# Performance work log

Hardware: AMD Instinct MI355X
Metric: run time of the kernel (lower is better)

## Reference

```python
import jax, jax.numpy as jnp
import numpy as np

PI = 3.141592653589793
DET_THRESHOLD = 0.25
MAX_DET = 100
REG_HEAD = 4
DEPTH_MEAN = 28.01  # smoke_coder.depth_ref[0]
DIM_REF = (3.88, 1.63, 1.53)  # smoke_coder.dim_ref[0] (l, h, w)


def setup_inputs() -> dict:
    key = jax.random.key(0)
    k1, k2, k3, k4 = jax.random.split(key, 4)
    B, C, H, W = 32, 3, 256, 832  # stride-4 feature map of 3328x1024 images
    pred_heatmap = jax.random.uniform(k1, (B, C, H, W), dtype=jnp.float32)
    pred_regression = jax.random.normal(k2, (B, C + 1, H, W), dtype=jnp.float32) * 0.1  # REG_HEAD=4 channels
    trans_mat = jnp.tile(jnp.array([[0.25, 0.0, 0.0], [0.0, 0.25, 0.0], [0.0, 0.0, 1.0]], jnp.float32), (B, 1, 1))
    K_mat = jnp.tile(jnp.array([[2100.0, 0.0, 1664.0], [0.0, 2100.0, 512.0], [0.0, 0.0, 1.0]], jnp.float32), (B, 1, 1))
    size = jnp.tile(jnp.array([3328.0, 1024.0], jnp.float32), (B, 1))  # (img_w, img_h)
    h_cam = jax.random.uniform(k3, (B,), jnp.float32, 1.4, 2.0)
    dimensions = jax.random.uniform(k4, (B, 3), jnp.float32, 1.5, 4.0)
    return dict(pred_heatmap=pred_heatmap, pred_regression=pred_regression, trans_mat=trans_mat,
                K_mat=K_mat, size=size, h_cam=h_cam, dimensions=dimensions)


def reference(pred_heatmap, pred_regression, trans_mat, K_mat, size, h_cam, dimensions):
    B, C, H, W = pred_heatmap.shape
    K = MAX_DET
    # ---- nms_hm: 3x3 max-pool, keep local maxima ----
    hmax = jax.lax.reduce_window(pred_heatmap, -jnp.inf, jax.lax.max, (1, 1, 3, 3), (1, 1, 1, 1), 'SAME')
    heat = pred_heatmap * (hmax == pred_heatmap).astype(pred_heatmap.dtype)
    # ---- select_topk: per-class topk then global topk ----
    scores_c, inds_c = jax.lax.top_k(heat.reshape(B, C, H * W), K)  # [B,C,K]
    ys_c = (inds_c // W).astype(jnp.float32)
    xs_c = (inds_c % W).astype(jnp.float32)
    scores, topk_ind = jax.lax.top_k(scores_c.reshape(B, C * K), K)  # [B,K]
    clses = (topk_ind // K).astype(jnp.float32)
    inds = jnp.take_along_axis(inds_c.reshape(B, C * K), topk_ind, axis=1)
    ys = jnp.take_along_axis(ys_c.reshape(B, C * K), topk_ind, axis=1)
    xs = jnp.take_along_axis(xs_c.reshape(B, C * K), topk_ind, axis=1)
    feat = pred_regression.reshape(B, REG_HEAD, H * W).transpose(0, 2, 1)  # [B,HW,R]
    pois = jnp.take_along_axis(feat, inds[:, :, None], axis=1).reshape(-1, REG_HEAD)  # [B*K,R]
    log_dv_delta = pois[:, 0]
    off_u = pois[:, 1]
    ori = pois[:, 2:]
    # ---- feature points -> image points via inverse affine ----
    pts = jnp.stack([xs.reshape(-1), ys.reshape(-1)], axis=1)
    pts = pts + jnp.stack([off_u, jnp.zeros_like(off_u)], axis=1)
    pts_h = jnp.concatenate([pts, jnp.ones((pts.shape[0], 1), pts.dtype)], axis=1)  # [N,3]
    obj = jnp.repeat(jnp.arange(B), K)
    trans_inv = jnp.linalg.inv(trans_mat)[obj]  # [N,3,3]
    img_pts = jnp.einsum('nij,nj->ni', trans_inv, pts_h)[:, :2]
    # ---- per-object camera params ----
    Ks = K_mat[obj]
    h = h_cam[obj]
    kd = dimensions[obj]
    fx, fy, cx = Ks[:, 0, 0], Ks[:, 1, 1], Ks[:, 0, 2]
    dim_ref = jnp.array(DIM_REF, jnp.float32)
    dims = jnp.where(jnp.isfinite(kd), kd, dim_ref[None, :])
    # ---- geometric depth decode ----
    h_ref = h - dims[:, 1] / 2.0
    log_dv_ref = jnp.log(jnp.clip(fy * jnp.abs(h_ref), 1e-7, None) / DEPTH_MEAN)
    log_dv = jnp.clip(log_dv_ref + log_dv_delta, -4.0, 8.0)
    depths = jnp.clip(fy * jnp.abs(h_ref) * jnp.exp(-log_dv), 0.5, 120.0)
    px = (img_pts[:, 0] - cx) * depths / fx
    locs = jnp.stack([px, h, depths], axis=1)  # [N,3]
    # ---- decode_orientation (SMOKE) ----
    rays = jnp.arctan(locs[:, 0] / (locs[:, 2] + 1e-7))
    alphas = jnp.arctan(ori[:, 0] / (ori[:, 1] + 1e-7))
    alphas = alphas + jnp.where(ori[:, 1] >= 0, -PI / 2, PI / 2)
    rotys = alphas + rays
    rotys = jnp.where(rotys > PI, rotys - 2 * PI, rotys)
    rotys = jnp.where(rotys < -PI, rotys + 2 * PI, rotys)
    # ---- encode_box2d: build 3D corners, rotate, project, clamp ----
    cos, sin = jnp.cos(rotys), jnp.sin(rotys)
    cx8 = jnp.array([-0.5, 0.5, 0.5, 0.5, 0.5, -0.5, -0.5, -0.5], jnp.float32)
    cy8 = jnp.array([-1.0, -1.0, 0.0, 0.0, -1.0, -1.0, 0.0, 0.0], jnp.float32)
    cz8 = jnp.array([-0.5, -0.5, -0.5, 0.5, 0.5, 0.5, 0.5, -0.5], jnp.float32)
    xc = dims[:, 0:1] * cx8  # l
    yc = dims[:, 1:2] * cy8  # h
    zc = dims[:, 2:3] * cz8  # w
    bx = cos[:, None] * xc + sin[:, None] * zc
    bz = -sin[:, None] * xc + cos[:, None] * zc
    box3d = jnp.stack([bx, yc, bz], axis=1) + locs[:, :, None]  # [N,3,8]
    proj = jnp.einsum('nij,njk->nik', Ks, box3d)
    uv = proj[:, :2, :] / proj[:, 2:3, :]
    img_w = size.reshape(-1)[0]
    img_h = size.reshape(-1)[1]
    xmins = jnp.clip(jnp.min(uv[:, 0, :], axis=1), 0.0, img_w)
    xmaxs = jnp.clip(jnp.max(uv[:, 0, :], axis=1), 0.0, img_w)
    ymins = jnp.clip(jnp.min(uv[:, 1, :], axis=1), 0.0, img_h)
    ymaxs = jnp.clip(jnp.max(uv[:, 1, :], axis=1), 0.0, img_h)
    box2d = jnp.stack([xmins, ymins, xmaxs, ymaxs], axis=1)
    pred_dims = jnp.roll(dims, -1, axis=1)  # (l,h,w)->(h,w,l)
    result = jnp.concatenate([clses.reshape(-1, 1), alphas[:, None], box2d, pred_dims, locs,
                              rotys[:, None], scores.reshape(-1, 1)], axis=1)  # [N,14]
    # fixed-shape equivalent of boolean filtering: zero out rows below threshold
    keep = (result[:, -1] > DET_THRESHOLD).astype(result.dtype)
    return result * keep[:, None]
```

## Files before the change

kernel.cpp:

```cpp
#include <hip/hip_runtime.h>
#include <math.h>

#define B_ 32
#define C_ 3
#define H_ 256
#define W_ 832
#define HW_ (H_*W_)
#define NQ (W_/4)
#define K_ 100
#define RPB 16
#define PARTS (H_/RPB)
#define BLK 256
#define CAP 2048
#define NCAND (C_*PARTS*K_)
#define NB 2048
#define TIE_CAP 128
#define SEL_PASSES 6
#define QPW 62

typedef unsigned long long ull;

template<int N>
__device__ inline void bitonic_sort_desc(ull* s) {
    for (int k = 2; k <= N; k <<= 1) {
        for (int j = k >> 1; j > 0; j >>= 1) {
            __syncthreads();
            for (int i = threadIdx.x; i < N; i += BLK) {
                int ixj = i ^ j;
                if (ixj > i) {
                    ull a = s[i], b = s[ixj];
                    bool up = ((i & k) == 0);
                    if (up ? (a < b) : (a > b)) { s[i] = b; s[ixj] = a; }
                }
            }
        }
    }
    __syncthreads();
}

__device__ inline void find_digit(const unsigned* __restrict__ hist,
                                  unsigned* __restrict__ wtot,
                                  const int kneed,
                                  int* __restrict__ d_s,
                                  int* __restrict__ krem_s,
                                  int* __restrict__ m_s) {
    const int tid = threadIdx.x;
    const int lane = tid & 63;
    const int wid = tid >> 6;
    unsigned l[8];
    unsigned Ls = 0;
    #pragma unroll
    for (int j = 0; j < 8; ++j) { l[j] = hist[tid * 8 + j]; Ls += l[j]; }
    unsigned x = Ls;
    #pragma unroll
    for (int off = 1; off < 64; off <<= 1) {
        unsigned y = __shfl_down(x, off);
        if (lane + off < 64) x += y;
    }
    if (lane == 0) wtot[wid] = x;
    __syncthreads();
    unsigned tail = 0;
    #pragma unroll
    for (int w = 0; w < 4; ++w) if (w > wid) tail += wtot[w];
    unsigned s = x - Ls + tail;
    #pragma unroll
    for (int j = 7; j >= 0; --j) {
        const unsigned Sj = s + l[j];
        if (Sj >= (unsigned)kneed && s < (unsigned)kneed) {
            *d_s = tid * 8 + j;
            *krem_s = kneed - (int)s;
            *m_s = (int)l[j];
        }
        s = Sj;
    }
    __syncthreads();
}

__device__ inline void select_topk(const ull* __restrict__ buf, const int cnt,
                                   ull* __restrict__ dst,
                                   unsigned* __restrict__ hist,
                                   ull* __restrict__ tie,
                                   unsigned* __restrict__ wtot,
                                   int* __restrict__ sh) {
    const int tid = threadIdx.x;
    const int lane = tid & 63;
    if (tid == 0) sh[0] = 0;
    int kneed = K_;
    int pshift = 0;
    ull prefix = 0;
    for (int pass = 0; pass < SEL_PASSES; ++pass) {
        const int rs = 53 - 11 * pass;
        const int shift = (rs > 0) ? rs : 0;
        #pragma unroll
        for (int j = 0; j < NB / BLK; ++j) hist[tid + j * BLK] = 0u;
        if (tid == 0) sh[1] = 0;
        __syncthreads();
        if (pass == 0) {
            for (int i = tid; i < cnt; i += BLK) {
                const unsigned dg = (unsigned)(buf[i] >> shift) & 2047u;
                ull unclaimed = __ballot(1);
                while (unclaimed) {
                    const int leader = __ffsll((long long)unclaimed) - 1;
                    const unsigned ldg = __shfl(dg, leader);
                    const ull same = __ballot(dg == ldg);
                    if (lane == leader)
                        atomicAdd(&hist[ldg], (unsigned)__popcll(same));
                    unclaimed &= ~same;
                }
            }
        } else {
            for (int i = tid; i < cnt; i += BLK) {
                const ull key = buf[i];
                if ((key >> pshift) != prefix) continue;
                atomicAdd(&hist[(unsigned)(key >> shift) & 2047u], 1u);
            }
        }
        __syncthreads();
        find_digit(hist, wtot, kneed, &sh[2], &sh[3], &sh[4]);
        const int d = sh[2], krem = sh[3], m = sh[4];
        const bool last = (m <= TIE_CAP) || (pass == SEL_PASSES - 1);
        for (int i = tid; i < cnt; i += BLK) {
            const ull key = buf[i];
            if (pass > 0 && (key >> pshift) != prefix) continue;
            const int dg = (int)((unsigned)(key >> shift) & 2047u);
            if (dg > d) {
                dst[atomicAdd(&sh[0], 1)] = key;
            } else if (last && dg == d) {
                const int p = atomicAdd(&sh[1], 1);
                if (p < TIE_CAP) tie[p] = key;
            }
        }
        __syncthreads();
        if (last) {
            const int n1 = K_ - krem;
            if (sh[1] <= TIE_CAP) {
                const int mm = sh[1];
                for (int i = tid; i < mm; i += BLK) {
                    const ull key = tie[i];
                    int r = 0;
                    for (int j = 0; j < mm; ++j) r += (tie[j] > key) ? 1 : 0;
                    if (r < krem) dst[n1 + r] = key;
                }
            } else {
                for (int i = tid; i < krem; i += BLK) dst[n1 + i] = tie[0];
            }
            __syncthreads();
            return;
        }
        prefix = (prefix << 11) | (ull)(unsigned)d;
        pshift = shift;
        kneed = krem;
    }
}

__global__ void __launch_bounds__(BLK) topk_part_kernel(
        const float* __restrict__ heat, ull* __restrict__ part_out) {
    const int chan = blockIdx.x / PARTS;
    const int c    = chan % C_;
    const int part = blockIdx.x % PARTS;
    const float* __restrict__ hp = heat + (size_t)chan * HW_;
    const int r0 = part * RPB;
    const int tid = threadIdx.x;
    const int lane = tid & 63;
    const int wid = tid >> 6;

    const int q = QPW * wid + lane - 1;
    const bool ghost = (q < 0) || (q >= NQ);
    const int qc = (q < 0) ? 0 : ((q >= NQ) ? NQ - 1 : q);
    const bool emitter = (lane >= 1) && (lane <= QPW) && !ghost;

    __shared__ unsigned hist[NB];
    __shared__ ull buf[CAP];
    __shared__ ull tie[TIE_CAP];
    __shared__ unsigned wtot[4];
    __shared__ int cnt;
    __shared__ int selsh[5];
    if (tid == 0) cnt = 0;

    float4 R[6];
    #pragma unroll
    for (int j = 0; j < 6; ++j) {
        int row = r0 - 1 + j;
        row = (row < 0) ? 0 : ((row > H_ - 1) ? H_ - 1 : row);
        R[j] = reinterpret_cast<const float4*>(hp + (size_t)row * W_)[qc];
    }
    __syncthreads();

    #pragma unroll
    for (int r = 0; r < RPB; ++r) {
        const int y = r0 + r;
        const float4 ra = R[r % 6];
        const float4 rb = R[(r + 1) % 6];
        const float4 rc = R[(r + 2) % 6];
        if (r < RPB - 4) {
            const int yn = (y + 5 > H_ - 1) ? H_ - 1 : y + 5;
            R[r % 6] = reinterpret_cast<const float4*>(hp + (size_t)yn * W_)[qc];
        }

        float4 vm;
        vm.x = fmaxf(fmaxf(ra.x, rb.x), rc.x);
        vm.y = fmaxf(fmaxf(ra.y, rb.y), rc.y);
        vm.z = fmaxf(fmaxf(ra.z, rb.z), rc.z);
        vm.w = fmaxf(fmaxf(ra.w, rb.w), rc.w);
        if (ghost) { vm.x = vm.y = vm.z = vm.w = -INFINITY; }

        const float left  = __shfl_up(vm.w, 1);
        const float right = __shfl_down(vm.x, 1);

        const float vn[6] = {left, vm.x, vm.y, vm.z, vm.w, right};
        const float vv[4] = {rb.x, rb.y, rb.z, rb.w};
        ull m[4];
        bool pk[4];
        #pragma unroll
        for (int i = 0; i < 4; ++i) {
            pk[i] = emitter && (vv[i] >= vn[i]) && (vv[i] >= vn[i+1]) && (vv[i] >= vn[i+2]);
            m[i] = __ballot(pk[i]);
        }
        const int tot = (int)(__popcll(m[0]) + __popcll(m[1]) +
                              __popcll(m[2]) + __popcll(m[3]));
        if (tot) {
            int base = 0;
            if (lane == 0) base = atomicAdd(&cnt, tot);
            base = __shfl(base, 0);
            int off = 0;
            #pragma unroll
            for (int i = 0; i < 4; ++i) {
                if (pk[i]) {
                    const unsigned p = (unsigned)(y * W_ + q * 4 + i);
                    const unsigned tiek = ((unsigned)c << 18) | p;
                    const ull key = ((ull)__float_as_uint(vv[i]) << 32) | (ull)(~tiek);
                    const int rank = (int)__popcll(m[i] & ((1ULL << lane) - 1ULL));
                    const int pos = base + off + rank;
                    if (pos < CAP) buf[pos] = key;
                }
                off += (int)__popcll(m[i]);
            }
        }
    }
    __syncthreads();

    const int cc = (cnt < CAP) ? cnt : CAP;
    ull* o = part_out + (size_t)blockIdx.x * K_;

    if (cc <= K_) {
        for (int i = tid; i < cc; i += BLK) o[i] = buf[i];
        for (int i = cc + tid; i < K_; i += BLK) o[i] = 0ULL;
        return;
    }

    select_topk(buf, cc, o, hist, tie, wtot, selsh);
}

__global__ void __launch_bounds__(BLK) merge_geom_kernel(
        const ull* __restrict__ part_keys, const float* __restrict__ reg,
        const float* __restrict__ trans, const float* __restrict__ Km,
        const float* __restrict__ sz, const float* __restrict__ hcam,
        const float* __restrict__ dimen, float* __restrict__ out) {
    const int b = blockIdx.x;
    const int tid = threadIdx.x;
    __shared__ ull buf[NCAND];
    __shared__ unsigned hist[NB];
    __shared__ ull sel[128];
    __shared__ ull tie[TIE_CAP];
    __shared__ unsigned wtot[4];
    __shared__ int selsh[5];
    const ull* src = part_keys + (size_t)b * NCAND;
    for (int i = tid; i < NCAND; i += BLK) buf[i] = src[i];
    if (tid < 128) sel[tid] = 0ULL;
    __syncthreads();

    select_topk(buf, NCAND, sel, hist, tie, wtot, selsh);

    bitonic_sort_desc<128>(sel);

    for (int i = tid; i < K_; i += BLK) {
        const ull key = sel[i];
        const unsigned tiek = ~(unsigned)(key & 0xFFFFFFFFULL);
        const float score = __uint_as_float((unsigned)(key >> 32));
        const float clsf = (float)((tiek >> 18) & 3u);
        unsigned hw = tiek & 0x3FFFFu;
        if (hw >= HW_) hw = 0;
        const float xs = (float)(hw % W_);
        const float ys = (float)(hw / W_);

        const float* rg = reg + (size_t)b * 4 * HW_;
        const float delta = rg[hw];
        const float off_u = rg[HW_ + hw];
        const float ori0  = rg[2 * HW_ + hw];
        const float ori1  = rg[3 * HW_ + hw];

        const float* T = trans + b * 9;
        const float t00=T[0], t01=T[1], t02=T[2], t10=T[3], t11=T[4], t12=T[5],
                    t20=T[6], t21=T[7], t22=T[8];
        const float det3 = t00*(t11*t22 - t12*t21) - t01*(t10*t22 - t12*t20)
                         + t02*(t10*t21 - t11*t20);
        const float idt = 1.0f / det3;
        const float i00 = (t11*t22 - t12*t21)*idt;
        const float i01 = (t02*t21 - t01*t22)*idt;
        const float i02 = (t01*t12 - t02*t11)*idt;

        const float pu = xs + off_u;
        const float img_x = i00*pu + i01*ys + i02;

        const float* Kb = Km + b * 9;
        const float k00=Kb[0],k01=Kb[1],k02=Kb[2],k10=Kb[3],k11=Kb[4],k12=Kb[5],
                    k20=Kb[6],k21=Kb[7],k22=Kb[8];
        const float fx = k00, fy = k11, cx = k02;
        const float h = hcam[b];
        float d0 = dimen[b*3+0], d1 = dimen[b*3+1], d2 = dimen[b*3+2];
        if (!isfinite(d0)) d0 = 3.88f;
        if (!isfinite(d1)) d1 = 1.63f;
        if (!isfinite(d2)) d2 = 1.53f;

        const float h_ref = h - d1 * 0.5f;
        const float fyh = fy * fabsf(h_ref);
        const float log_dv_ref = logf(fmaxf(fyh, 1e-7f) / 28.01f);
        const float log_dv = fminf(fmaxf(log_dv_ref + delta, -4.0f), 8.0f);
        const float depth = fminf(fmaxf(fyh * expf(-log_dv), 0.5f), 120.0f);
        const float px = (img_x - cx) * depth / fx;

        const float PI_F  = 3.14159265358979323846f;
        const float ray = atanf(px / (depth + 1e-7f));
        float alpha = atanf(ori0 / (ori1 + 1e-7f));
        alpha += (ori1 >= 0.0f) ? -1.5707963267948966f : 1.5707963267948966f;
        float roty = alpha + ray;
        if (roty >  PI_F) roty -= 6.283185307179586f;
        if (roty < -PI_F) roty += 6.283185307179586f;

        const float cosr = cosf(roty), sinr = sinf(roty);
        const float cx8[8] = {-0.5f, 0.5f, 0.5f, 0.5f, 0.5f,-0.5f,-0.5f,-0.5f};
        const float cy8[8] = {-1.0f,-1.0f, 0.0f, 0.0f,-1.0f,-1.0f, 0.0f, 0.0f};
        const float cz8[8] = {-0.5f,-0.5f,-0.5f, 0.5f, 0.5f, 0.5f, 0.5f,-0.5f};
        float umin = 1e30f, umax = -1e30f, vmin = 1e30f, vmax = -1e30f;
        #pragma unroll
        for (int j = 0; j < 8; ++j) {
            const float xc = d0 * cx8[j];
            const float yc = d1 * cy8[j];
            const float zc = d2 * cz8[j];
            const float X = cosr*xc + sinr*zc + px;
            const float Y = yc + h;
            const float Z = -sinr*xc + cosr*zc + depth;
            const float w = k20*X + k21*Y + k22*Z;
            const float u = (k00*X + k01*Y + k02*Z) / w;
            const float v = (k10*X + k11*Y + k12*Z) / w;
            umin = fminf(umin, u); umax = fmaxf(umax, u);
            vmin = fminf(vmin, v); vmax = fmaxf(vmax, v);
        }
        const float img_w = sz[0], img_h = sz[1];
        const float xmin = fminf(fmaxf(umin, 0.0f), img_w);
        const float xmax = fminf(fmaxf(umax, 0.0f), img_w);
        const float ymin = fminf(fmaxf(vmin, 0.0f), img_h);
        const float ymax = fminf(fmaxf(vmax, 0.0f), img_h);

        const float keep = (score > 0.25f) ? 1.0f : 0.0f;
        float* o = out + (size_t)(b * K_ + i) * 14;
        o[0]  = clsf  * keep;
        o[1]  = alpha * keep;
        o[2]  = xmin  * keep;
        o[3]  = ymin  * keep;
        o[4]  = xmax  * keep;
        o[5]  = ymax  * keep;
        o[6]  = d1    * keep;
        o[7]  = d2    * keep;
        o[8]  = d0    * keep;
        o[9]  = px    * keep;
        o[10] = h     * keep;
        o[11] = depth * keep;
        o[12] = roty  * keep;
        o[13] = score * keep;
    }
}

extern "C" void kernel_launch(void* const* d_in, const int* in_sizes, int n_in,
                              void* d_out, int out_size, void* d_ws, size_t ws_size,
                              hipStream_t stream) {
    const float* heat  = (const float*)d_in[0];
    const float* reg   = (const float*)d_in[1];
    const float* trans = (const float*)d_in[2];
    const float* Kmat  = (const float*)d_in[3];
    const float* sz    = (const float*)d_in[4];
    const float* hcam  = (const float*)d_in[5];
    const float* dimen = (const float*)d_in[6];
    float* out = (float*)d_out;

    ull* part_keys = (ull*)d_ws;

    topk_part_kernel<<<B_ * C_ * PARTS, BLK, 0, stream>>>(heat, part_keys);
    merge_geom_kernel<<<B_, BLK, 0, stream>>>(
        part_keys, reg, trans, Kmat, sz, hcam, dimen, out);
}
```

Before: 239.9 us.

## Replace per-tile top-k with global hot/rest peak bucketing and single merge select

Drops the per-block radix top-k selection in the peak-finding kernel. Each block now scatters its local-maximum keys into per-batch global buffers, split into a 'hot' bucket (score >= 0.99) and a 'rest' bucket, using a packed 64-bit atomic counter. The merge kernel runs its radix select only over the hot bucket when that bucket holds at least K entries, and falls back to both buckets otherwise, so the result stays exact. In exchange, every peak key is now written to global memory, and the change adds a memset launch and global atomics per batch.

```diff
diff --git a/kernel.cpp b/kernel.cpp
--- a/kernel.cpp
+++ b/kernel.cpp
@@ -12,11 +12,13 @@
 #define PARTS (H_/RPB)
 #define BLK 256
 #define CAP 2048
-#define NCAND (C_*PARTS*K_)
 #define NB 2048
 #define TIE_CAP 128
 #define SEL_PASSES 6
 #define QPW 62
+#define HCAP 16384
+#define RCAP 98304
+#define T_HOT 0.99f
 
 typedef unsigned long long ull;
 
@@ -76,14 +78,21 @@
     __syncthreads();
 }
 
-__device__ inline void select_topk(const ull* __restrict__ buf, const int cnt,
-                                   ull* __restrict__ dst,
-                                   unsigned* __restrict__ hist,
-                                   ull* __restrict__ tie,
-                                   unsigned* __restrict__ wtot,
-                                   int* __restrict__ sh) {
+__device__ inline ull fetch2(const ull* __restrict__ A, const int na,
+                             const ull* __restrict__ Bp, const int i) {
+    return (i < na) ? A[i] : Bp[i - na];
+}
+
+__device__ inline void select_topk_g(const ull* __restrict__ A, const int na,
+                                     const ull* __restrict__ Bp, const int nb,
+                                     ull* __restrict__ dst,
+                                     unsigned* __restrict__ hist,
+                                     ull* __restrict__ tie,
+                                     unsigned* __restrict__ wtot,
+                                     int* __restrict__ sh) {
     const int tid = threadIdx.x;
     const int lane = tid & 63;
+    const int cnt = na + nb;
     if (tid == 0) sh[0] = 0;
     int kneed = K_;
     int pshift = 0;
@@ -97,7 +106,7 @@
         __syncthreads();
         if (pass == 0) {
             for (int i = tid; i < cnt; i += BLK) {
-                const unsigned dg = (unsigned)(buf[i] >> shift) & 2047u;
+                const unsigned dg = (unsigned)(fetch2(A, na, Bp, i) >> shift) & 2047u;
                 ull unclaimed = __ballot(1);
                 while (unclaimed) {
                     const int leader = __ffsll((long long)unclaimed) - 1;
@@ -110,7 +119,7 @@
             }
         } else {
             for (int i = tid; i < cnt; i += BLK) {
-                const ull key = buf[i];
+                const ull key = fetch2(A, na, Bp, i);
                 if ((key >> pshift) != prefix) continue;
                 atomicAdd(&hist[(unsigned)(key >> shift) & 2047u], 1u);
             }
@@ -120,7 +129,7 @@
         const int d = sh[2], krem = sh[3], m = sh[4];
         const bool last = (m <= TIE_CAP) || (pass == SEL_PASSES - 1);
         for (int i = tid; i < cnt; i += BLK) {
-            const ull key = buf[i];
+            const ull key = fetch2(A, na, Bp, i);
             if (pass > 0 && (key >> pshift) != prefix) continue;
             const int dg = (int)((unsigned)(key >> shift) & 2047u);
             if (dg > d) {
@@ -153,10 +162,12 @@
     }
 }
 
-__global__ void __launch_bounds__(BLK) topk_part_kernel(
-        const float* __restrict__ heat, ull* __restrict__ part_out) {
+__global__ void __launch_bounds__(BLK) peaks_kernel(
+        const float* __restrict__ heat, ull* __restrict__ hot,
+        ull* __restrict__ rest, ull* __restrict__ cnt64) {
     const int chan = blockIdx.x / PARTS;
     const int c    = chan % C_;
+    const int b    = chan / C_;
     const int part = blockIdx.x % PARTS;
     const float* __restrict__ hp = heat + (size_t)chan * HW_;
     const int r0 = part * RPB;
@@ -169,13 +180,9 @@
     const int qc = (q < 0) ? 0 : ((q >= NQ) ? NQ - 1 : q);
     const bool emitter = (lane >= 1) && (lane <= QPW) && !ghost;
 
-    __shared__ unsigned hist[NB];
-    __shared__ ull buf[CAP];
-    __shared__ ull tie[TIE_CAP];
-    __shared__ unsigned wtot[4];
-    __shared__ int cnt;
-    __shared__ int selsh[5];
-    if (tid == 0) cnt = 0;
+    __shared__ ull sbuf[CAP];
+    __shared__ int scnt;
+    if (tid == 0) scnt = 0;
 
     float4 R[6];
     #pragma unroll
@@ -220,7 +227,7 @@
                               __popcll(m[2]) + __popcll(m[3]));
         if (tot) {
             int base = 0;
-            if (lane == 0) base = atomicAdd(&cnt, tot);
+            if (lane == 0) base = atomicAdd(&scnt, tot);
             base = __shfl(base, 0);
             int off = 0;
             #pragma unroll
@@ -231,7 +238,7 @@
                     const ull key = ((ull)__float_as_uint(vv[i]) << 32) | (ull)(~tiek);
                     const int rank = (int)__popcll(m[i] & ((1ULL << lane) - 1ULL));
                     const int pos = base + off + rank;
-                    if (pos < CAP) buf[pos] = key;
+                    if (pos < CAP) sbuf[pos] = key;
                 }
                 off += (int)__popcll(m[i]);
             }
@@ -239,37 +246,80 @@
     }
     __syncthreads();
 
-    const int cc = (cnt < CAP) ? cnt : CAP;
-    ull* o = part_out + (size_t)blockIdx.x * K_;
-
-    if (cc <= K_) {
-        for (int i = tid; i < cc; i += BLK) o[i] = buf[i];
-        for (int i = cc + tid; i < K_; i += BLK) o[i] = 0ULL;
-        return;
-    }
-
-    select_topk(buf, cc, o, hist, tie, wtot, selsh);
+    const int cc = (scnt < CAP) ? scnt : CAP;
+
+    ull* __restrict__ hb = hot  + (size_t)b * HCAP;
+    ull* __restrict__ rb2 = rest + (size_t)b * RCAP;
+    for (int i0 = wid * 64; i0 < cc; i0 += BLK) {
+        const int i = i0 + lane;
+        const bool valid = i < cc;
+        const ull key = valid ? sbuf[i] : 0ULL;
+        const float v = __uint_as_float((unsigned)(key >> 32));
+        const bool hotf  = valid && (v >= T_HOT);
+        const bool restf = valid && !hotf;
+        const ull mh = __ballot(hotf);
+        const ull mr = __ballot(restf);
+        const int th = (int)__popcll(mh), tr = (int)__popcll(mr);
+        int bh = 0, br = 0;
+        if (lane == 0) {
+            const ull ret = atomicAdd(cnt64 + b, ((ull)(unsigned)th << 32) | (unsigned)tr);
+            bh = (int)(ret >> 32);
+            br = (int)(ret & 0xffffffffu);
+        }
+        bh = __shfl(bh, 0);
+        br = __shfl(br, 0);
+        if (hotf) {
+            const int pos = bh + (int)__popcll(mh & ((1ULL << lane) - 1ULL));
+            if (pos < HCAP) {
+                hb[pos] = key;
+            } else {
+                const unsigned p2 = (unsigned)(atomicAdd(cnt64 + b, 1ULL) & 0xffffffffu);
+                if ((int)p2 < RCAP) rb2[p2] = key;
+            }
+        }
+        if (restf) {
+            const int pos = br + (int)__popcll(mr & ((1ULL << lane) - 1ULL));
+            if (pos < RCAP) rb2[pos] = key;
+        }
+    }
 }
 
 __global__ void __launch_bounds__(BLK) merge_geom_kernel(
-        const ull* __restrict__ part_keys, const float* __restrict__ reg,
+        const ull* __restrict__ hot, const ull* __restrict__ rest,
+        const ull* __restrict__ cnt64, const float* __restrict__ reg,
         const float* __restrict__ trans, const float* __restrict__ Km,
         const float* __restrict__ sz, const float* __restrict__ hcam,
         const float* __restrict__ dimen, float* __restrict__ out) {
     const int b = blockIdx.x;
     const int tid = threadIdx.x;
-    __shared__ ull buf[NCAND];
     __shared__ unsigned hist[NB];
     __shared__ ull sel[128];
     __shared__ ull tie[TIE_CAP];
     __shared__ unsigned wtot[4];
     __shared__ int selsh[5];
-    const ull* src = part_keys + (size_t)b * NCAND;
-    for (int i = tid; i < NCAND; i += BLK) buf[i] = src[i];
+
+    const ull cw = cnt64[b];
+    const int ch_raw = (int)(cw >> 32);
+    const int cr_raw = (int)(cw & 0xffffffffu);
+    const ull* A  = hot  + (size_t)b * HCAP;
+    const ull* Bp = rest + (size_t)b * RCAP;
+    int na, nb2;
+    if (ch_raw >= K_ && ch_raw <= HCAP) {
+        na = ch_raw; nb2 = 0;
+    } else {
+        na  = (ch_raw < HCAP) ? ch_raw : HCAP;
+        nb2 = (cr_raw < RCAP) ? cr_raw : RCAP;
+    }
+    const int cnt = na + nb2;
+
     if (tid < 128) sel[tid] = 0ULL;
     __syncthreads();
 
-    select_topk(buf, NCAND, sel, hist, tie, wtot, selsh);
+    if (cnt <= K_) {
+        for (int i = tid; i < cnt; i += BLK) sel[i] = fetch2(A, na, Bp, i);
+    } else {
+        select_topk_g(A, na, Bp, nb2, sel, hist, tie, wtot, selsh);
+    }
 
     bitonic_sort_desc<128>(sel);
 
@@ -383,9 +433,15 @@
     const float* dimen = (const float*)d_in[6];
     float* out = (float*)d_out;
 
-    ull* part_keys = (ull*)d_ws;
-
-    topk_part_kernel<<<B_ * C_ * PARTS, BLK, 0, stream>>>(heat, part_keys);
+    char* ws = (char*)d_ws;
+    ull* cnt64 = (ull*)ws;
+    ws += 256;
+    ull* hot = (ull*)ws;
+    ws += (size_t)B_ * HCAP * sizeof(ull);
+    ull* rest = (ull*)ws;
+
+    hipMemsetAsync(cnt64, 0, B_ * sizeof(ull), stream);
+    peaks_kernel<<<B_ * C_ * PARTS, BLK, 0, stream>>>(heat, hot, rest, cnt64);
     merge_geom_kernel<<<B_, BLK, 0, stream>>>(
-        part_keys, reg, trans, Kmat, sz, hcam, dimen, out);
-}
+        hot, rest, cnt64, reg, trans, Kmat, sz, hcam, dimen, out);
+}
```

After: 451.1 us. 1.88x slower.
